# Optimization experiments

Hardware: AMD Instinct MI355X
Metric: run time of the kernel (lower is better)

The kernel has to match this reference:

```python
import jax, jax.numpy as jnp
import numpy as np

KH = KW = 3  # kernel size for both convs


def conv2d_valid(x, w, b):
    # x: [B,C,H,W], w: [O,C,KH,KW], VALID padding, stride 1 (matches nn.Conv2d(3,18,3))
    y = jax.lax.conv_general_dilated(x, w, window_strides=(1, 1), padding='VALID',
                                     dimension_numbers=('NCHW', 'OIHW', 'NCHW'))
    return y + b[None, :, None, None]


def deform_conv2d(x, offset, w, b):
    # Faithful torchvision deform_conv2d: stride 1, pad 0, dilation 1, 1 group, 1 offset group.
    B, C, H, W = x.shape
    O = w.shape[0]
    Ho, Wo = offset.shape[2], offset.shape[3]
    K = KH * KW
    # offset layout: [B, 2*K, Ho, Wo], per-tap (dy, dx) interleaved, taps row-major
    off = offset.reshape(B, K, 2, Ho, Wo)
    dy, dx = off[:, :, 0], off[:, :, 1]                      # [B,K,Ho,Wo]
    ky = jnp.repeat(jnp.arange(KH), KW).astype(x.dtype)       # [K] tap row
    kx = jnp.tile(jnp.arange(KW), KH).astype(x.dtype)         # [K] tap col
    py = dy + jnp.arange(Ho, dtype=x.dtype)[None, None, :, None] + ky[None, :, None, None]
    px = dx + jnp.arange(Wo, dtype=x.dtype)[None, None, None, :] + kx[None, :, None, None]

    y0 = jnp.floor(py); x0 = jnp.floor(px)
    wy = py - y0; wx = px - x0                                # bilinear fractions
    y0i = y0.astype(jnp.int32); x0i = x0.astype(jnp.int32)

    x_flat = x.reshape(B, C, H * W)

    def corner(yi, xi):
        valid = ((yi >= 0) & (yi < H) & (xi >= 0) & (xi < W)).astype(x.dtype)  # zero pad outside
        idx = jnp.clip(yi, 0, H - 1) * W + jnp.clip(xi, 0, W - 1)              # [B,K,Ho,Wo]
        g = jax.vmap(lambda xf, ix: xf[:, ix])(x_flat, idx)                    # [B,C,K,Ho,Wo]
        return g * valid[:, None]

    val = (corner(y0i, x0i)         * ((1 - wy) * (1 - wx))[:, None]
         + corner(y0i, x0i + 1)     * ((1 - wy) * wx)[:, None]
         + corner(y0i + 1, x0i)     * (wy * (1 - wx))[:, None]
         + corner(y0i + 1, x0i + 1) * (wy * wx)[:, None])     # [B,C,K,Ho,Wo]

    out = jnp.einsum('bckhw,ock->bohw', val, w.reshape(O, C, K))
    return out + b[None, :, None, None]


def setup_inputs() -> dict:
    key = jax.random.key(0)
    k1, k2, k3, k4, k5 = jax.random.split(key, 5)
    B, C, H, W = 16, 3, 384, 384
    x = jax.random.normal(k1, (B, C, H, W), dtype=jnp.float32)
    # offset conv: Conv2d(3, 18, 3); scale down so learned offsets stay moderate
    conv_w = jax.random.normal(k2, (18, 3, KH, KW), dtype=jnp.float32) * 0.05
    conv_b = jax.random.normal(k3, (18,), dtype=jnp.float32) * 0.05
    # deform conv: DeformConv2d(3, 3, 3)
    dcn_w = jax.random.normal(k4, (3, 3, KH, KW), dtype=jnp.float32) * (1.0 / np.sqrt(3 * KH * KW))
    dcn_b = jax.random.normal(k5, (3,), dtype=jnp.float32) * 0.05
    return {'x': x, 'conv_w': conv_w, 'conv_b': conv_b, 'dcn_w': dcn_w, 'dcn_b': dcn_b}


def reference(x, conv_w, conv_b, dcn_w, dcn_b):
    offset = conv2d_valid(x, conv_w, conv_b)   # [B,18,H-2,W-2]
    return deform_conv2d(x, offset, dcn_w, dcn_b)  # [B,3,H-2,W-2]
```

## Files before the change

kernel.cpp:

```cpp
#include <hip/hip_runtime.h>

#define BATCH 16
#define CIN   3
#define H     384
#define W     384
#define HW    (H * W)
#define HO    382
#define WO    382
#define OFFC  18
#define OOUT  3
#define KTAPS 9

#define PAD   2
#define HP    (H + 2 * PAD)
#define WP    (W + 2 * PAD)

#define WPK_FLOATS 588

#define NXCD 8

typedef float vf2 __attribute__((ext_vector_type(2)));
struct F3 { float a, b, c; };

static __device__ __forceinline__ vf2 splat2(float s) { vf2 r; r.x = s; r.y = s; return r; }

static __device__ __forceinline__ unsigned f2bf(float f) {
    const unsigned u = __float_as_uint(f);
    return (u + 0x7fffu + ((u >> 16) & 1u)) >> 16;
}
static __device__ __forceinline__ float bf_lo(unsigned d) { return __uint_as_float(d << 16); }
static __device__ __forceinline__ float bf_hi(unsigned d) { return __uint_as_float(d & 0xffff0000u); }

__global__ __launch_bounds__(256)
void pack_bf16_kernel(const float* __restrict__ x,
                      const float* __restrict__ conv_w,
                      const float* __restrict__ conv_b,
                      const float* __restrict__ dcn_w,
                      const float* __restrict__ dcn_b,
                      uint2* __restrict__ xt,
                      float* __restrict__ wpk)
{
    const int b  = blockIdx.y;
    const int r2 = blockIdx.x * 256 + threadIdx.x;

    if (blockIdx.x == 0 && b == 0) {
        for (int i = threadIdx.x; i < WPK_FLOATS; i += 256) {
            float v;
            if (i < 486) {
                const int k    = i / 54;
                const int r    = i - k * 54;
                const int idx  = r >> 1;
                const int half = r & 1;
                v = conv_w[(2 * k + half) * 27 + idx];
            } else if (i < 504) {
                v = conv_b[i - 486];
            } else if (i < 558) {
                const int r    = i - 504;
                const int ck   = r >> 1;
                const int half = r & 1;
                v = dcn_w[half * 27 + ck];
            } else if (i < 585) {
                v = dcn_w[2 * 27 + (i - 558)];
            } else if (i < 587) {
                v = dcn_b[i - 585];
            } else {
                v = dcn_b[2];
            }
            wpk[i] = v;
        }
    }

    if (r2 >= HP * WP) return;
    const int ry = r2 / WP;
    const int rx = r2 - ry * WP;
    const int yi = ry - PAD;
    const int xi = rx - PAD;
    uint2 v = make_uint2(0u, 0u);
    if ((unsigned)yi < (unsigned)H && (unsigned)xi < (unsigned)W) {
        const float* xb = x + (size_t)b * (CIN * HW);
        const int p = yi * W + xi;
        v.x = f2bf(xb[p]) | (f2bf(xb[HW + p]) << 16);
        v.y = f2bf(xb[2 * HW + p]);
    }
    xt[(size_t)b * (HP * WP) + r2] = v;
}

__global__ __launch_bounds__(256, 5)
void deform_bf16_kernel(const float* __restrict__ x,
                        const uint2* __restrict__ xt,
                        const float* __restrict__ wpk,
                        float* __restrict__ out)
{
    const int total = BATCH * HO * WO;
    const int nwg   = (total + 255) / 256;
    const int q     = nwg / NXCD;
    const int r     = nwg % NXCD;

    const int orig = blockIdx.x;
    const int xcd  = orig & (NXCD - 1);
    const int idx  = orig >> 3;
    const int base = (xcd < r) ? xcd * (q + 1) : r * (q + 1) + (xcd - r) * q;
    const int wg   = base + idx;

    const int gid = wg * 256 + threadIdx.x;
    if (gid >= total) return;

    const int wo  = gid % WO;
    const int tmp = gid / WO;
    const int ho  = tmp % HO;
    const int b   = tmp / HO;

    const vf2*   pk_cw = (const vf2*)wpk;
    const vf2*   pk_cb = (const vf2*)(wpk + 486);
    const vf2*   pk_dw = (const vf2*)(wpk + 504);
    const float* dw2   = wpk + 558;

    const float* xb  = x  + (size_t)b * (CIN * HW);
    const uint2* xtb = xt + (size_t)b * (HP * WP);

    float xp[CIN][3][3];
    #pragma unroll
    for (int c = 0; c < CIN; ++c) {
        const float* xc = xb + c * HW + ho * W + wo;
        #pragma unroll
        for (int i = 0; i < 3; ++i)
            #pragma unroll
            for (int j = 0; j < 3; ++j)
                xp[c][i][j] = xc[i * W + j];
    }

    vf2 off2[KTAPS];
    #pragma unroll
    for (int k = 0; k < KTAPS; ++k) {
        vf2 a = pk_cb[k];
        #pragma unroll
        for (int c = 0; c < CIN; ++c)
            #pragma unroll
            for (int i = 0; i < 3; ++i)
                #pragma unroll
                for (int j = 0; j < 3; ++j)
                    a = __builtin_elementwise_fma(pk_cw[k * 27 + c * 9 + i * 3 + j],
                                                  splat2(xp[c][i][j]), a);
        off2[k] = a;
    }

    vf2   acc01 = *(const vf2*)(wpk + 585);
    float acc2  = wpk[587];

    #pragma unroll
    for (int k = 0; k < KTAPS; ++k) {
        const int ky = k / 3;
        const int kx = k % 3;
        const vf2 o = off2[k];
        vf2 f;
        f.x = floorf(o.x);
        f.y = floorf(o.y);
        const vf2 w  = o - f;
        const vf2 cw = splat2(1.f) - w;

        int iy = (int)f.x + (ho + ky + PAD);
        int ix = (int)f.y + (wo + kx + PAD);
        iy = min(max(iy, 0), HP - 2);
        ix = min(max(ix, 0), WP - 2);

        const uint2* base2 = xtb + iy * WP + ix;
        const uint2 q00 = base2[0];
        const uint2 q01 = base2[1];
        const uint2 q10 = base2[WP];
        const uint2 q11 = base2[WP + 1];

        const float w00 = cw.x * cw.y;
        const float w01 = cw.x * w.y;
        const float w10 = w.x * cw.y;
        const float w11 = w.x * w.y;

        vf2 c00, c01, c10, c11;
        c00.x = bf_lo(q00.x); c00.y = bf_hi(q00.x);
        c01.x = bf_lo(q01.x); c01.y = bf_hi(q01.x);
        c10.x = bf_lo(q10.x); c10.y = bf_hi(q10.x);
        c11.x = bf_lo(q11.x); c11.y = bf_hi(q11.x);
        vf2 s01 = c00 * splat2(w00);
        s01 = __builtin_elementwise_fma(c01, splat2(w01), s01);
        s01 = __builtin_elementwise_fma(c10, splat2(w10), s01);
        s01 = __builtin_elementwise_fma(c11, splat2(w11), s01);

        float s2 = bf_lo(q00.y) * w00;
        s2 = fmaf(bf_lo(q01.y), w01, s2);
        s2 = fmaf(bf_lo(q10.y), w10, s2);
        s2 = fmaf(bf_lo(q11.y), w11, s2);

        acc01 = __builtin_elementwise_fma(pk_dw[0 * 9 + k], splat2(s01.x), acc01);
        acc01 = __builtin_elementwise_fma(pk_dw[1 * 9 + k], splat2(s01.y), acc01);
        acc01 = __builtin_elementwise_fma(pk_dw[2 * 9 + k], splat2(s2),    acc01);
        acc2 = fmaf(dw2[0 * 9 + k], s01.x, acc2);
        acc2 = fmaf(dw2[1 * 9 + k], s01.y, acc2);
        acc2 = fmaf(dw2[2 * 9 + k], s2,    acc2);
    }

    const int obase = b * (OOUT * HO * WO) + ho * WO + wo;
    __builtin_nontemporal_store(acc01.x, out + obase);
    __builtin_nontemporal_store(acc01.y, out + obase + HO * WO);
    __builtin_nontemporal_store(acc2,    out + obase + 2 * HO * WO);
}

__global__ __launch_bounds__(256)
void chw_to_hwc_kernel(const float* __restrict__ x, float* __restrict__ xt)
{
    const int gid = blockIdx.x * 256 + threadIdx.x;
    if (gid >= BATCH * HW) return;
    const int b = gid / HW;
    const int p = gid - b * HW;
    const float* xb = x + (size_t)b * (CIN * HW);
    F3 v;
    v.a = xb[p];
    v.b = xb[HW + p];
    v.c = xb[2 * HW + p];
    *(F3*)(xt + (size_t)gid * 3) = v;
}

__global__ __launch_bounds__(256)
void deform_hwc_kernel(const float* __restrict__ xt,
                       const float* __restrict__ conv_w,
                       const float* __restrict__ conv_b,
                       const float* __restrict__ dcn_w,
                       const float* __restrict__ dcn_b,
                       float* __restrict__ out)
{
    const int total = BATCH * HO * WO;
    const int gid = blockIdx.x * 256 + threadIdx.x;
    if (gid >= total) return;

    const int wo  = gid % WO;
    const int tmp = gid / WO;
    const int ho  = tmp % HO;
    const int b   = tmp / HO;

    const float* xtb = xt + (size_t)b * (HW * 3);

    F3 xp[3][3];
    #pragma unroll
    for (int i = 0; i < 3; ++i)
        #pragma unroll
        for (int j = 0; j < 3; ++j)
            xp[i][j] = *(const F3*)(xtb + (size_t)((ho + i) * W + (wo + j)) * 3);

    float off[OFFC];
    #pragma unroll
    for (int o = 0; o < OFFC; ++o) {
        float a = conv_b[o];
        #pragma unroll
        for (int i = 0; i < 3; ++i)
            #pragma unroll
            for (int j = 0; j < 3; ++j) {
                a = fmaf(conv_w[o * 27 + 0 * 9 + i * 3 + j], xp[i][j].a, a);
                a = fmaf(conv_w[o * 27 + 1 * 9 + i * 3 + j], xp[i][j].b, a);
                a = fmaf(conv_w[o * 27 + 2 * 9 + i * 3 + j], xp[i][j].c, a);
            }
        off[o] = a;
    }

    float acc0 = dcn_b[0];
    float acc1 = dcn_b[1];
    float acc2 = dcn_b[2];

    #pragma unroll
    for (int k = 0; k < KTAPS; ++k) {
        const int ky = k / 3;
        const int kx = k % 3;
        const float py = off[2 * k]     + (float)(ho + ky);
        const float px = off[2 * k + 1] + (float)(wo + kx);
        const float y0f = floorf(py);
        const float x0f = floorf(px);
        const float wy = py - y0f;
        const float wx = px - x0f;
        const int y0 = (int)y0f;
        const int x0 = (int)x0f;
        const int y1 = y0 + 1;
        const int x1 = x0 + 1;
        const bool vy0 = (unsigned)y0 < (unsigned)H;
        const bool vy1 = (unsigned)y1 < (unsigned)H;
        const bool vx0 = (unsigned)x0 < (unsigned)W;
        const bool vx1 = (unsigned)x1 < (unsigned)W;
        const int cy0 = min(max(y0, 0), H - 1);
        const int cy1 = min(max(y1, 0), H - 1);
        const int cx0 = min(max(x0, 0), W - 1);
        const int cx1 = min(max(x1, 0), W - 1);
        const float w00 = (vy0 && vx0) ? (1.f - wy) * (1.f - wx) : 0.f;
        const float w01 = (vy0 && vx1) ? (1.f - wy) * wx         : 0.f;
        const float w10 = (vy1 && vx0) ? wy * (1.f - wx)         : 0.f;
        const float w11 = (vy1 && vx1) ? wy * wx                 : 0.f;

        const F3 v00 = *(const F3*)(xtb + (size_t)(cy0 * W + cx0) * 3);
        const F3 v01 = *(const F3*)(xtb + (size_t)(cy0 * W + cx1) * 3);
        const F3 v10 = *(const F3*)(xtb + (size_t)(cy1 * W + cx0) * 3);
        const F3 v11 = *(const F3*)(xtb + (size_t)(cy1 * W + cx1) * 3);

        float s0 = v00.a * w00; s0 = fmaf(v01.a, w01, s0); s0 = fmaf(v10.a, w10, s0); s0 = fmaf(v11.a, w11, s0);
        float s1 = v00.b * w00; s1 = fmaf(v01.b, w01, s1); s1 = fmaf(v10.b, w10, s1); s1 = fmaf(v11.b, w11, s1);
        float s2 = v00.c * w00; s2 = fmaf(v01.c, w01, s2); s2 = fmaf(v10.c, w10, s2); s2 = fmaf(v11.c, w11, s2);

        acc0 = fmaf(dcn_w[0 * 27 + 0 * 9 + k], s0, acc0);
        acc0 = fmaf(dcn_w[0 * 27 + 1 * 9 + k], s1, acc0);
        acc0 = fmaf(dcn_w[0 * 27 + 2 * 9 + k], s2, acc0);
        acc1 = fmaf(dcn_w[1 * 27 + 0 * 9 + k], s0, acc1);
        acc1 = fmaf(dcn_w[1 * 27 + 1 * 9 + k], s1, acc1);
        acc1 = fmaf(dcn_w[1 * 27 + 2 * 9 + k], s2, acc1);
        acc2 = fmaf(dcn_w[2 * 27 + 0 * 9 + k], s0, acc2);
        acc2 = fmaf(dcn_w[2 * 27 + 1 * 9 + k], s1, acc2);
        acc2 = fmaf(dcn_w[2 * 27 + 2 * 9 + k], s2, acc2);
    }

    const int obase = b * (OOUT * HO * WO) + ho * WO + wo;
    __builtin_nontemporal_store(acc0, out + obase);
    __builtin_nontemporal_store(acc1, out + obase + HO * WO);
    __builtin_nontemporal_store(acc2, out + obase + 2 * HO * WO);
}

__global__ __launch_bounds__(256)
void deform_fused_kernel(const float* __restrict__ x,
                         const float* __restrict__ conv_w,
                         const float* __restrict__ conv_b,
                         const float* __restrict__ dcn_w,
                         const float* __restrict__ dcn_b,
                         float* __restrict__ out)
{
    __shared__ float s_cw[OFFC * 27];
    __shared__ float s_cb[OFFC];
    __shared__ float s_dw[OOUT * 27];
    __shared__ float s_db[OOUT];

    const int t = threadIdx.x;
    for (int i = t; i < OFFC * 27; i += 256) s_cw[i] = conv_w[i];
    if (t < OFFC)      s_cb[t] = conv_b[t];
    if (t < OOUT * 27) s_dw[t] = dcn_w[t];
    if (t < OOUT)      s_db[t] = dcn_b[t];
    __syncthreads();

    const int total = BATCH * HO * WO;
    const int gid = blockIdx.x * 256 + t;
    if (gid >= total) return;

    const int wo  = gid % WO;
    const int tmp = gid / WO;
    const int ho  = tmp % HO;
    const int b   = tmp / HO;

    const float* xb = x + b * (CIN * HW);

    float xp[CIN][3][3];
    #pragma unroll
    for (int c = 0; c < CIN; ++c) {
        const float* xc = xb + c * HW + ho * W + wo;
        #pragma unroll
        for (int i = 0; i < 3; ++i)
            #pragma unroll
            for (int j = 0; j < 3; ++j)
                xp[c][i][j] = xc[i * W + j];
    }

    float off[OFFC];
    #pragma unroll
    for (int o = 0; o < OFFC; ++o) {
        float a = s_cb[o];
        const float* wv = &s_cw[o * 27];
        #pragma unroll
        for (int c = 0; c < CIN; ++c)
            #pragma unroll
            for (int i = 0; i < 3; ++i)
                #pragma unroll
                for (int j = 0; j < 3; ++j)
                    a = fmaf(wv[c * 9 + i * 3 + j], xp[c][i][j], a);
        off[o] = a;
    }

    float a0 = s_db[0], a1 = s_db[1], a2 = s_db[2];

    #pragma unroll
    for (int k = 0; k < KTAPS; ++k) {
        const int ky = k / 3;
        const int kx = k % 3;
        const float py = off[2 * k]     + (float)(ho + ky);
        const float px = off[2 * k + 1] + (float)(wo + kx);
        const float y0f = floorf(py);
        const float x0f = floorf(px);
        const float wy = py - y0f;
        const float wx = px - x0f;
        const int y0 = (int)y0f;
        const int x0 = (int)x0f;
        const int y1 = y0 + 1;
        const int x1 = x0 + 1;
        const bool vy0 = (unsigned)y0 < (unsigned)H;
        const bool vy1 = (unsigned)y1 < (unsigned)H;
        const bool vx0 = (unsigned)x0 < (unsigned)W;
        const bool vx1 = (unsigned)x1 < (unsigned)W;
        const int cy0 = min(max(y0, 0), H - 1);
        const int cy1 = min(max(y1, 0), H - 1);
        const int cx0 = min(max(x0, 0), W - 1);
        const int cx1 = min(max(x1, 0), W - 1);
        const float w00 = (vy0 && vx0) ? (1.f - wy) * (1.f - wx) : 0.f;
        const float w01 = (vy0 && vx1) ? (1.f - wy) * wx         : 0.f;
        const float w10 = (vy1 && vx0) ? wy * (1.f - wx)         : 0.f;
        const float w11 = (vy1 && vx1) ? wy * wx                 : 0.f;
        const int i00 = cy0 * W + cx0;
        const int i01 = cy0 * W + cx1;
        const int i10 = cy1 * W + cx0;
        const int i11 = cy1 * W + cx1;
        #pragma unroll
        for (int c = 0; c < CIN; ++c) {
            const float* xc = xb + c * HW;
            float s = xc[i00] * w00;
            s = fmaf(xc[i01], w01, s);
            s = fmaf(xc[i10], w10, s);
            s = fmaf(xc[i11], w11, s);
            a0 = fmaf(s_dw[0 * 27 + c * 9 + k], s, a0);
            a1 = fmaf(s_dw[1 * 27 + c * 9 + k], s, a1);
            a2 = fmaf(s_dw[2 * 27 + c * 9 + k], s, a2);
        }
    }

    const int obase = b * (OOUT * HO * WO) + ho * WO + wo;
    __builtin_nontemporal_store(a0, out + obase);
    __builtin_nontemporal_store(a1, out + obase + HO * WO);
    __builtin_nontemporal_store(a2, out + obase + 2 * HO * WO);
}

extern "C" void kernel_launch(void* const* d_in, const int* in_sizes, int n_in,
                              void* d_out, int out_size, void* d_ws, size_t ws_size,
                              hipStream_t stream) {
    const float* x      = (const float*)d_in[0];
    const float* conv_w = (const float*)d_in[1];
    const float* conv_b = (const float*)d_in[2];
    const float* dcn_w  = (const float*)d_in[3];
    const float* dcn_b  = (const float*)d_in[4];
    float* out = (float*)d_out;

    const int total = BATCH * HO * WO;
    const size_t xt_bytes = (size_t)BATCH * HP * WP * sizeof(uint2);
    const size_t need_bf = xt_bytes + WPK_FLOATS * sizeof(float);
    const size_t need3   = (size_t)BATCH * HW * 3 * sizeof(float);

    if (ws_size >= need_bf) {
        uint2* xt = (uint2*)d_ws;
        float* wpk = (float*)((char*)d_ws + xt_bytes);
        dim3 pack_grid((HP * WP + 255) / 256, BATCH);
        pack_bf16_kernel<<<pack_grid, 256, 0, stream>>>(
            x, conv_w, conv_b, dcn_w, dcn_b, xt, wpk);
        deform_bf16_kernel<<<(total + 255) / 256, 256, 0, stream>>>(x, xt, wpk, out);
    } else if (ws_size >= need3) {
        float* xt = (float*)d_ws;
        chw_to_hwc_kernel<<<(BATCH * HW + 255) / 256, 256, 0, stream>>>(x, xt);
        deform_hwc_kernel<<<(total + 255) / 256, 256, 0, stream>>>(
            xt, conv_w, conv_b, dcn_w, dcn_b, out);
    } else {
        deform_fused_kernel<<<(total + 255) / 256, 256, 0, stream>>>(
            x, conv_w, conv_b, dcn_w, dcn_b, out);
    }
}
```

Before: 139.1 us.

## Compute two adjacent output pixels per thread with vectorized patch loads

```diff
diff --git a/kernel.cpp b/kernel.cpp
--- a/kernel.cpp
+++ b/kernel.cpp
@@ -18,8 +18,13 @@
 #define WPK_FLOATS 588
 
 #define NXCD 8
+#define PPROW 191
+#define PPIMG (HO * PPROW)
+#define PBLK  286
+#define NWG2  (BATCH * PBLK)
 
 typedef float vf2 __attribute__((ext_vector_type(2)));
+typedef float vf4 __attribute__((ext_vector_type(4)));
 struct F3 { float a, b, c; };
 
 static __device__ __forceinline__ vf2 splat2(float s) { vf2 r; r.x = s; r.y = s; return r; }
@@ -85,30 +90,23 @@
     xt[(size_t)b * (HP * WP) + r2] = v;
 }
 
-__global__ __launch_bounds__(256, 5)
+__global__ __launch_bounds__(256, 4)
 void deform_bf16_kernel(const float* __restrict__ x,
                         const uint2* __restrict__ xt,
                         const float* __restrict__ wpk,
                         float* __restrict__ out)
 {
-    const int total = BATCH * HO * WO;
-    const int nwg   = (total + 255) / 256;
-    const int q     = nwg / NXCD;
-    const int r     = nwg % NXCD;
-
     const int orig = blockIdx.x;
-    const int xcd  = orig & (NXCD - 1);
-    const int idx  = orig >> 3;
-    const int base = (xcd < r) ? xcd * (q + 1) : r * (q + 1) + (xcd - r) * q;
-    const int wg   = base + idx;
-
-    const int gid = wg * 256 + threadIdx.x;
-    if (gid >= total) return;
-
-    const int wo  = gid % WO;
-    const int tmp = gid / WO;
-    const int ho  = tmp % HO;
-    const int b   = tmp / HO;
+    const int wg   = (orig & (NXCD - 1)) * (NWG2 / NXCD) + (orig >> 3);
+
+    const int b   = wg / PBLK;
+    const int pbk = wg - b * PBLK;
+
+    const int tp = pbk * 256 + threadIdx.x;
+    if (tp >= PPIMG) return;
+    const int ho  = tp / PPROW;
+    const int wp_ = tp - ho * PPROW;
+    const int wo0 = wp_ * 2;
 
     const vf2*   pk_cw = (const vf2*)wpk;
     const vf2*   pk_cb = (const vf2*)(wpk + 486);
@@ -118,89 +116,104 @@
     const float* xb  = x  + (size_t)b * (CIN * HW);
     const uint2* xtb = xt + (size_t)b * (HP * WP);
 
-    float xp[CIN][3][3];
+    vf4 xq[CIN][3];
     #pragma unroll
     for (int c = 0; c < CIN; ++c) {
-        const float* xc = xb + c * HW + ho * W + wo;
+        const float* xc = xb + c * HW + ho * W + wo0;
         #pragma unroll
         for (int i = 0; i < 3; ++i)
-            #pragma unroll
-            for (int j = 0; j < 3; ++j)
-                xp[c][i][j] = xc[i * W + j];
-    }
-
-    vf2 off2[KTAPS];
+            __builtin_memcpy(&xq[c][i], xc + i * W, 16);
+    }
+
+    vf2 offA[KTAPS], offB[KTAPS];
     #pragma unroll
     for (int k = 0; k < KTAPS; ++k) {
-        vf2 a = pk_cb[k];
+        vf2 aA = pk_cb[k];
+        vf2 aB = pk_cb[k];
         #pragma unroll
         for (int c = 0; c < CIN; ++c)
             #pragma unroll
             for (int i = 0; i < 3; ++i)
                 #pragma unroll
-                for (int j = 0; j < 3; ++j)
-                    a = __builtin_elementwise_fma(pk_cw[k * 27 + c * 9 + i * 3 + j],
-                                                  splat2(xp[c][i][j]), a);
-        off2[k] = a;
-    }
-
-    vf2   acc01 = *(const vf2*)(wpk + 585);
-    float acc2  = wpk[587];
+                for (int j = 0; j < 3; ++j) {
+                    const vf2 w = pk_cw[k * 27 + c * 9 + i * 3 + j];
+                    aA = __builtin_elementwise_fma(w, splat2(xq[c][i][j]),     aA);
+                    aB = __builtin_elementwise_fma(w, splat2(xq[c][i][j + 1]), aB);
+                }
+        offA[k] = aA;
+        offB[k] = aB;
+    }
+
+    vf2   accA01 = *(const vf2*)(wpk + 585);
+    float accA2  = wpk[587];
+    vf2   accB01 = accA01;
+    float accB2  = accA2;
 
     #pragma unroll
     for (int k = 0; k < KTAPS; ++k) {
         const int ky = k / 3;
         const int kx = k % 3;
-        const vf2 o = off2[k];
-        vf2 f;
-        f.x = floorf(o.x);
-        f.y = floorf(o.y);
-        const vf2 w  = o - f;
-        const vf2 cw = splat2(1.f) - w;
-
-        int iy = (int)f.x + (ho + ky + PAD);
-        int ix = (int)f.y + (wo + kx + PAD);
-        iy = min(max(iy, 0), HP - 2);
-        ix = min(max(ix, 0), WP - 2);
-
-        const uint2* base2 = xtb + iy * WP + ix;
-        const uint2 q00 = base2[0];
-        const uint2 q01 = base2[1];
-        const uint2 q10 = base2[WP];
-        const uint2 q11 = base2[WP + 1];
-
-        const float w00 = cw.x * cw.y;
-        const float w01 = cw.x * w.y;
-        const float w10 = w.x * cw.y;
-        const float w11 = w.x * w.y;
-
-        vf2 c00, c01, c10, c11;
-        c00.x = bf_lo(q00.x); c00.y = bf_hi(q00.x);
-        c01.x = bf_lo(q01.x); c01.y = bf_hi(q01.x);
-        c10.x = bf_lo(q10.x); c10.y = bf_hi(q10.x);
-        c11.x = bf_lo(q11.x); c11.y = bf_hi(q11.x);
-        vf2 s01 = c00 * splat2(w00);
-        s01 = __builtin_elementwise_fma(c01, splat2(w01), s01);
-        s01 = __builtin_elementwise_fma(c10, splat2(w10), s01);
-        s01 = __builtin_elementwise_fma(c11, splat2(w11), s01);
-
-        float s2 = bf_lo(q00.y) * w00;
-        s2 = fmaf(bf_lo(q01.y), w01, s2);
-        s2 = fmaf(bf_lo(q10.y), w10, s2);
-        s2 = fmaf(bf_lo(q11.y), w11, s2);
-
-        acc01 = __builtin_elementwise_fma(pk_dw[0 * 9 + k], splat2(s01.x), acc01);
-        acc01 = __builtin_elementwise_fma(pk_dw[1 * 9 + k], splat2(s01.y), acc01);
-        acc01 = __builtin_elementwise_fma(pk_dw[2 * 9 + k], splat2(s2),    acc01);
-        acc2 = fmaf(dw2[0 * 9 + k], s01.x, acc2);
-        acc2 = fmaf(dw2[1 * 9 + k], s01.y, acc2);
-        acc2 = fmaf(dw2[2 * 9 + k], s2,    acc2);
-    }
-
-    const int obase = b * (OOUT * HO * WO) + ho * WO + wo;
-    __builtin_nontemporal_store(acc01.x, out + obase);
-    __builtin_nontemporal_store(acc01.y, out + obase + HO * WO);
-    __builtin_nontemporal_store(acc2,    out + obase + 2 * HO * WO);
+
+        #pragma unroll
+        for (int p = 0; p < 2; ++p) {
+            const vf2 o = (p == 0) ? offA[k] : offB[k];
+            vf2&   acc01 = (p == 0) ? accA01 : accB01;
+            float& acc2  = (p == 0) ? accA2  : accB2;
+            const int wo = wo0 + p;
+
+            vf2 f;
+            f.x = floorf(o.x);
+            f.y = floorf(o.y);
+            const vf2 w  = o - f;
+            const vf2 cw = splat2(1.f) - w;
+
+            int iy = (int)f.x + (ho + ky + PAD);
+            int ix = (int)f.y + (wo + kx + PAD);
+            iy = min(max(iy, 0), HP - 2);
+            ix = min(max(ix, 0), WP - 2);
+
+            const uint2* base2 = xtb + iy * WP + ix;
+            const uint2 q00 = base2[0];
+            const uint2 q01 = base2[1];
+            const uint2 q10 = base2[WP];
+            const uint2 q11 = base2[WP + 1];
+
+            const float w00 = cw.x * cw.y;
+            const float w01 = cw.x * w.y;
+            const float w10 = w.x * cw.y;
+            const float w11 = w.x * w.y;
+
+            vf2 c00, c01, c10, c11;
+            c00.x = bf_lo(q00.x); c00.y = bf_hi(q00.x);
+            c01.x = bf_lo(q01.x); c01.y = bf_hi(q01.x);
+            c10.x = bf_lo(q10.x); c10.y = bf_hi(q10.x);
+            c11.x = bf_lo(q11.x); c11.y = bf_hi(q11.x);
+            vf2 s01 = c00 * splat2(w00);
+            s01 = __builtin_elementwise_fma(c01, splat2(w01), s01);
+            s01 = __builtin_elementwise_fma(c10, splat2(w10), s01);
+            s01 = __builtin_elementwise_fma(c11, splat2(w11), s01);
+
+            float s2 = bf_lo(q00.y) * w00;
+            s2 = fmaf(bf_lo(q01.y), w01, s2);
+            s2 = fmaf(bf_lo(q10.y), w10, s2);
+            s2 = fmaf(bf_lo(q11.y), w11, s2);
+
+            acc01 = __builtin_elementwise_fma(pk_dw[0 * 9 + k], splat2(s01.x), acc01);
+            acc01 = __builtin_elementwise_fma(pk_dw[1 * 9 + k], splat2(s01.y), acc01);
+            acc01 = __builtin_elementwise_fma(pk_dw[2 * 9 + k], splat2(s2),    acc01);
+            acc2 = fmaf(dw2[0 * 9 + k], s01.x, acc2);
+            acc2 = fmaf(dw2[1 * 9 + k], s01.y, acc2);
+            acc2 = fmaf(dw2[2 * 9 + k], s2,    acc2);
+        }
+    }
+
+    const int obase = b * (OOUT * HO * WO) + ho * WO + wo0;
+    vf2 st0; st0.x = accA01.x; st0.y = accB01.x;
+    vf2 st1; st1.x = accA01.y; st1.y = accB01.y;
+    vf2 st2; st2.x = accA2;    st2.y = accB2;
+    __builtin_nontemporal_store(st0, (vf2*)(out + obase));
+    __builtin_nontemporal_store(st1, (vf2*)(out + obase + HO * WO));
+    __builtin_nontemporal_store(st2, (vf2*)(out + obase + 2 * HO * WO));
 }
 
 __global__ __launch_bounds__(256)
@@ -445,7 +458,7 @@
         dim3 pack_grid((HP * WP + 255) / 256, BATCH);
         pack_bf16_kernel<<<pack_grid, 256, 0, stream>>>(
             x, conv_w, conv_b, dcn_w, dcn_b, xt, wpk);
-        deform_bf16_kernel<<<(total + 255) / 256, 256, 0, stream>>>(x, xt, wpk, out);
+        deform_bf16_kernel<<<NWG2, 256, 0, stream>>>(x, xt, wpk, out);
     } else if (ws_size >= need3) {
         float* xt = (float*)d_ws;
         chw_to_hwc_kernel<<<(BATCH * HW + 255) / 256, 256, 0, stream>>>(x, xt);
```

After: 138.5 us. No clear change (-0.4%).
